# Kernel tuning notes

Hardware: AMD Instinct MI355X
Metric: run time of the kernel (lower is better)

The kernel has to match this reference:

```python
import jax, jax.numpy as jnp
import numpy as np

N = 30000      # nodes
E = 480000     # edges (no self loops; GATConv adds them)
IN = 256       # in_features
OUT = 128      # out_features == per-head channels (concat=False)
H = 4          # heads
NEG_SLOPE = 0.2


def setup_inputs() -> dict:
    key = jax.random.key(0)
    k = jax.random.split(key, 6)
    x = jax.random.normal(k[0], (N, IN), dtype=jnp.float32)
    src = jax.random.randint(k[1], (E,), 0, N, dtype=jnp.int32)
    # guarantee no self loops (GATConv would strip them before re-adding)
    off = jax.random.randint(k[2], (E,), 1, N, dtype=jnp.int32)
    dst = (src + off) % N
    edge_index = jnp.stack([src, dst])  # [2, E]
    W = jax.random.normal(k[3], (IN, H * OUT), dtype=jnp.float32) / np.float32(np.sqrt(IN))
    att_src = jax.random.normal(k[4], (H, OUT), dtype=jnp.float32) / np.float32(np.sqrt(OUT))
    att_dst = jax.random.normal(k[5], (H, OUT), dtype=jnp.float32) / np.float32(np.sqrt(OUT))
    bias = jnp.zeros((OUT,), dtype=jnp.float32)
    return {"x": x, "edge_index": edge_index, "W": W,
            "att_src": att_src, "att_dst": att_dst, "bias": bias}


def reference(x, edge_index, W, att_src, att_dst, bias):
    n = x.shape[0]
    # dense projection -> per-head features [N, H, C]
    h = (x @ W).reshape(n, H, OUT)
    a_s = jnp.einsum('nhc,hc->nh', h, att_src)  # [N, H]
    a_d = jnp.einsum('nhc,hc->nh', h, att_dst)  # [N, H]
    # add self loops (GATConv default add_self_loops=True)
    loop = jnp.arange(n, dtype=edge_index.dtype)
    src = jnp.concatenate([edge_index[0], loop])  # [Et]
    dst = jnp.concatenate([edge_index[1], loop])  # [Et]
    # per-edge attention logits + LeakyReLU
    alpha = jax.nn.leaky_relu(a_s[src] + a_d[dst], NEG_SLOPE)  # [Et, H]
    # segment softmax over incoming edges of each dst node
    amax = jax.ops.segment_max(alpha, dst, num_segments=n)      # [N, H]
    ex = jnp.exp(alpha - amax[dst])
    denom = jax.ops.segment_sum(ex, dst, num_segments=n)        # [N, H]
    w = ex / denom[dst]                                          # [Et, H]
    # gather source features, weight, scatter-add to dst
    msg = h[src] * w[:, :, None]                                 # [Et, H, C]
    out = jax.ops.segment_sum(msg, dst, num_segments=n)          # [N, H, C]
    # concat=False -> mean over heads, then bias, then module's tanh
    out = out.mean(axis=1) + bias                                # [N, C]
    return jnp.tanh(out)
```

## Files before the change

### kernel.cpp

```cpp
#include <hip/hip_runtime.h>
#include <math.h>

#define IN_F   256
#define OUT_F  128
#define HEADS  4
#define HD     (HEADS * OUT_F)
#define K2     1024
#define NEG    0.2f
#define CAP    64

typedef __attribute__((ext_vector_type(8))) short short8;
typedef __attribute__((ext_vector_type(4))) float f32x4;

typedef __attribute__((address_space(1))) const void* gp_t;
typedef __attribute__((address_space(3))) void* lp_t;

static __device__ __forceinline__ ushort f2bf(float f) {
    union { float f; unsigned u; } v; v.f = f;
    unsigned r = (v.u + 0x7FFFu + ((v.u >> 16) & 1u)) >> 16;
    return (ushort)r;
}
static __device__ __forceinline__ float bflo(unsigned u) {
    union { unsigned u; float f; } v; v.u = u << 16; return v.f;
}
static __device__ __forceinline__ float bfhi(unsigned u) {
    union { unsigned u; float f; } v; v.u = u & 0xFFFF0000u; return v.f;
}

__global__ __launch_bounds__(256) void prep(const float* __restrict__ W,
                                            const float* __restrict__ att_src,
                                            const float* __restrict__ att_dst,
                                            const int* __restrict__ src,
                                            const int* __restrict__ dst,
                                            ushort* __restrict__ WT2,
                                            float* __restrict__ va_s,
                                            float* __restrict__ va_d,
                                            int* __restrict__ cursor,
                                            int* __restrict__ table,
                                            int n_edges) {
    const int b = blockIdx.x;
    const int tid = threadIdx.x;
    if (b < 512) {
        int idx = b * 256 + tid;
        int cout = idx >> 10, kk = idx & 1023;
        int h = kk >> 8, c = kk & 255;
        WT2[idx] = f2bf(W[(size_t)c * HD + h * OUT_F + cout]);
    } else if (b < 768) {
        const int lane = tid & 63;
        const int p = (b - 512) * 4 + (tid >> 6);
        const int h = p >> 8;
        const int k = p & 255;
        const float* wr = W + (size_t)k * HD + h * OUT_F;
        float w0 = wr[lane], w1 = wr[lane + 64];
        float s0 = att_src[h * OUT_F + lane], s1 = att_src[h * OUT_F + lane + 64];
        float d0 = att_dst[h * OUT_F + lane], d1 = att_dst[h * OUT_F + lane + 64];
        float ss = w0 * s0 + w1 * s1;
        float sd = w0 * d0 + w1 * d1;
#pragma unroll
        for (int off = 32; off > 0; off >>= 1) {
            ss += __shfl_xor(ss, off, 64);
            sd += __shfl_xor(sd, off, 64);
        }
        if (lane == 0) { va_s[p] = ss; va_d[p] = sd; }
    } else {
        int e = (b - 768) * 256 + tid;
        if (e < n_edges) {
            int d = dst[e];
            int r = atomicAdd(&cursor[d], 1);
            if (r < CAP) table[(size_t)d * CAP + r] = src[e];
        }
    }
}

__global__ __launch_bounds__(256) void fused_x(const float* __restrict__ X,
                                               const float* __restrict__ va_s,
                                               const float* __restrict__ va_d,
                                               ushort* __restrict__ Xb,
                                               float* __restrict__ a_s,
                                               float* __restrict__ a_d,
                                               int n_nodes) {
    const int lane = threadIdx.x & 63;
    const int node = blockIdx.x * 4 + (threadIdx.x >> 6);
    if (node >= n_nodes) return;
    float4 v = *(const float4*)(X + (size_t)node * IN_F + lane * 4);
    ushort4 o; o.x = f2bf(v.x); o.y = f2bf(v.y); o.z = f2bf(v.z); o.w = f2bf(v.w);
    *(ushort4*)(Xb + (size_t)node * IN_F + lane * 4) = o;

    float ps[HEADS], pd[HEADS];
#pragma unroll
    for (int hd = 0; hd < HEADS; ++hd) {
        float4 s4 = *(const float4*)(va_s + hd * IN_F + lane * 4);
        float4 d4 = *(const float4*)(va_d + hd * IN_F + lane * 4);
        ps[hd] = v.x * s4.x + v.y * s4.y + v.z * s4.z + v.w * s4.w;
        pd[hd] = v.x * d4.x + v.y * d4.y + v.z * d4.z + v.w * d4.w;
    }
#pragma unroll
    for (int off = 32; off > 0; off >>= 1) {
#pragma unroll
        for (int hd = 0; hd < HEADS; ++hd) {
            ps[hd] += __shfl_xor(ps[hd], off, 64);
            pd[hd] += __shfl_xor(pd[hd], off, 64);
        }
    }
    if (lane == 0) {
        float4 s4 = make_float4(ps[0], ps[1], ps[2], ps[3]);
        float4 d4 = make_float4(pd[0], pd[1], pd[2], pd[3]);
        *(float4*)(a_s + node * 4) = s4;
        *(float4*)(a_d + node * 4) = d4;
    }
}

#define ACC8(U, WE)                                                         \
    {                                                                       \
        float f0 = bflo((U).x), f1 = bfhi((U).x);                           \
        float f2 = bflo((U).y), f3 = bfhi((U).y);                           \
        acc[0][0] = fmaf((WE).x, f0, acc[0][0]);                            \
        acc[0][1] = fmaf((WE).x, f1, acc[0][1]);                            \
        acc[0][2] = fmaf((WE).x, f2, acc[0][2]);                            \
        acc[0][3] = fmaf((WE).x, f3, acc[0][3]);                            \
        acc[1][0] = fmaf((WE).y, f0, acc[1][0]);                            \
        acc[1][1] = fmaf((WE).y, f1, acc[1][1]);                            \
        acc[1][2] = fmaf((WE).y, f2, acc[1][2]);                            \
        acc[1][3] = fmaf((WE).y, f3, acc[1][3]);                            \
        acc[2][0] = fmaf((WE).z, f0, acc[2][0]);                            \
        acc[2][1] = fmaf((WE).z, f1, acc[2][1]);                            \
        acc[2][2] = fmaf((WE).z, f2, acc[2][2]);                            \
        acc[2][3] = fmaf((WE).z, f3, acc[2][3]);                            \
        acc[3][0] = fmaf((WE).w, f0, acc[3][0]);                            \
        acc[3][1] = fmaf((WE).w, f1, acc[3][1]);                            \
        acc[3][2] = fmaf((WE).w, f2, acc[3][2]);                            \
        acc[3][3] = fmaf((WE).w, f3, acc[3][3]);                            \
    }

#define GATHER8(E, D0, D1, D2, D3, D4, D5, D6, D7)                          \
    {                                                                       \
        int t0 = __shfl(sreg, (E) + 0, 64);                                 \
        int t1 = __shfl(sreg, (E) + 1, 64);                                 \
        int t2 = __shfl(sreg, (E) + 2, 64);                                 \
        int t3 = __shfl(sreg, (E) + 3, 64);                                 \
        int t4 = __shfl(sreg, (E) + 4, 64);                                 \
        int t5 = __shfl(sreg, (E) + 5, 64);                                 \
        int t6 = __shfl(sreg, (E) + 6, 64);                                 \
        int t7 = __shfl(sreg, (E) + 7, 64);                                 \
        D0 = xb2[(size_t)t0 * 64 + lane];                                   \
        D1 = xb2[(size_t)t1 * 64 + lane];                                   \
        D2 = xb2[(size_t)t2 * 64 + lane];                                   \
        D3 = xb2[(size_t)t3 * 64 + lane];                                   \
        D4 = xb2[(size_t)t4 * 64 + lane];                                   \
        D5 = xb2[(size_t)t5 * 64 + lane];                                   \
        D6 = xb2[(size_t)t6 * 64 + lane];                                   \
        D7 = xb2[(size_t)t7 * 64 + lane];                                   \
    }

__global__ __launch_bounds__(256) void gat_agg(const ushort* __restrict__ Xb,
                                               const float* __restrict__ a_s,
                                               const float* __restrict__ a_d,
                                               const int* __restrict__ cursor,
                                               const int* __restrict__ table,
                                               ushort* __restrict__ Zb,
                                               int n_nodes) {
    __shared__ float4 wse[4][CAP];
    const int lane = threadIdx.x & 63;
    const int wid  = threadIdx.x >> 6;
    int n = blockIdx.x * 4 + wid;
    const bool valid = n < n_nodes;
    if (!valid) n = n_nodes - 1;
    int deg = cursor[n]; if (deg > CAP) deg = CAP;
    const int* row = table + (size_t)n * CAP;
    const bool act = lane < deg;
    int sreg = act ? row[lane] : n;

    const uint2* xb2 = (const uint2*)Xb;
    uint2 uself = xb2[(size_t)n * 64 + lane];

    const int ngroups = (deg + 7) >> 3;
    uint2 ua0, ua1, ua2, ua3, ua4, ua5, ua6, ua7;
    if (ngroups > 0) GATHER8(0, ua0, ua1, ua2, ua3, ua4, ua5, ua6, ua7);

    const float4 ad4 = *(const float4*)(a_d + n * 4);
    const float4 as4 = *(const float4*)(a_s + n * 4);
    const float ad[4] = {ad4.x, ad4.y, ad4.z, ad4.w};
    float aself[4];
    {
        const float asn[4] = {as4.x, as4.y, as4.z, as4.w};
#pragma unroll
        for (int hd = 0; hd < 4; ++hd) {
            float al0 = asn[hd] + ad[hd];
            aself[hd] = al0 > 0.f ? al0 : NEG * al0;
        }
    }
    float al[4];
    {
        float4 av = *(const float4*)(a_s + (size_t)sreg * 4);
        const float as_[4] = {av.x, av.y, av.z, av.w};
#pragma unroll
        for (int hd = 0; hd < 4; ++hd) {
            float a = as_[hd] + ad[hd];
            a = a > 0.f ? a : NEG * a;
            al[hd] = act ? a : -1e30f;
        }
    }
    float m[4];
#pragma unroll
    for (int hd = 0; hd < 4; ++hd) m[hd] = al[hd];
#pragma unroll
    for (int off = 32; off > 0; off >>= 1)
#pragma unroll
        for (int hd = 0; hd < 4; ++hd)
            m[hd] = fmaxf(m[hd], __shfl_xor(m[hd], off, 64));
#pragma unroll
    for (int hd = 0; hd < 4; ++hd) m[hd] = fmaxf(m[hd], aself[hd]);

    float w[4], den[4];
#pragma unroll
    for (int hd = 0; hd < 4; ++hd) {
        w[hd] = act ? __expf(al[hd] - m[hd]) : 0.f;
        den[hd] = w[hd];
    }
#pragma unroll
    for (int off = 32; off > 0; off >>= 1)
#pragma unroll
        for (int hd = 0; hd < 4; ++hd)
            den[hd] += __shfl_xor(den[hd], off, 64);

    float es[4], rdv[4];
#pragma unroll
    for (int hd = 0; hd < 4; ++hd) {
        es[hd] = __expf(aself[hd] - m[hd]);
        rdv[hd] = 1.f / (den[hd] + es[hd]);
    }

    wse[wid][lane] = make_float4(w[0], w[1], w[2], w[3]);
    __syncthreads();

    float acc[4][4];
    {
        float f0 = bflo(uself.x), f1 = bfhi(uself.x);
        float f2 = bflo(uself.y), f3 = bfhi(uself.y);
#pragma unroll
        for (int hd = 0; hd < 4; ++hd) {
            acc[hd][0] = es[hd] * f0;
            acc[hd][1] = es[hd] * f1;
            acc[hd][2] = es[hd] * f2;
            acc[hd][3] = es[hd] * f3;
        }
    }
#pragma unroll 1
    for (int g = 0; g < ngroups; ++g) {
        int e = g * 8;
        uint2 ub0, ub1, ub2, ub3, ub4, ub5, ub6, ub7;
        if (g + 1 < ngroups)
            GATHER8(e + 8, ub0, ub1, ub2, ub3, ub4, ub5, ub6, ub7);
        float4 w0 = wse[wid][e + 0]; float4 w1 = wse[wid][e + 1];
        float4 w2 = wse[wid][e + 2]; float4 w3 = wse[wid][e + 3];
        float4 w4 = wse[wid][e + 4]; float4 w5 = wse[wid][e + 5];
        float4 w6 = wse[wid][e + 6]; float4 w7 = wse[wid][e + 7];
        ACC8(ua0, w0); ACC8(ua1, w1); ACC8(ua2, w2); ACC8(ua3, w3);
        ACC8(ua4, w4); ACC8(ua5, w5); ACC8(ua6, w6); ACC8(ua7, w7);
        if (g + 1 < ngroups) {
            ua0 = ub0; ua1 = ub1; ua2 = ub2; ua3 = ub3;
            ua4 = ub4; ua5 = ub5; ua6 = ub6; ua7 = ub7;
        }
    }

    if (valid) {
        ushort* zr = Zb + (size_t)n * K2;
#pragma unroll
        for (int hd = 0; hd < 4; ++hd) {
            ushort4 z;
            z.x = f2bf(acc[hd][0] * rdv[hd]);
            z.y = f2bf(acc[hd][1] * rdv[hd]);
            z.z = f2bf(acc[hd][2] * rdv[hd]);
            z.w = f2bf(acc[hd][3] * rdv[hd]);
            *(ushort4*)(zr + hd * 256 + lane * 4) = z;
        }
    }
}

#define GBM 64
#define GBN 128
#define GBK 64

__global__ __launch_bounds__(256) void gemm2(const ushort* __restrict__ Zb,
                                             const ushort* __restrict__ WT2,
                                             const float* __restrict__ bias,
                                             float* __restrict__ out,
                                             int n_nodes) {
    __shared__ ushort As[GBM][GBK];
    __shared__ ushort Bs[GBN][GBK];
    const int tid = threadIdx.x;
    const int m0 = blockIdx.y * GBM;
    const int wave = tid >> 6, lane = tid & 63;
    const int wm = (wave & 1) * 32, wn = (wave >> 1) * 64;
    const int l15 = lane & 15, quad = lane >> 4;

    const int rr8 = lane >> 3;
    const int cg  = (lane & 7) ^ rr8;
    const ushort* gA0 = Zb + (size_t)(m0 + wave * 16 + rr8) * K2 + cg * 8;
    const ushort* gA1 = gA0 + 8 * K2;
    const ushort* gB0 = WT2 + (size_t)(wave * 32 + rr8) * K2 + cg * 8;
    const ushort* gB1 = gB0 + 8 * K2;
    const ushort* gB2 = gB0 + 16 * K2;
    const ushort* gB3 = gB0 + 24 * K2;
    ushort* lA0 = &As[wave * 16][0];
    ushort* lA1 = &As[wave * 16 + 8][0];
    ushort* lB0 = &Bs[wave * 32][0];
    ushort* lB1 = &Bs[wave * 32 + 8][0];
    ushort* lB2 = &Bs[wave * 32 + 16][0];
    ushort* lB3 = &Bs[wave * 32 + 24][0];

    f32x4 acc[2][4];
#pragma unroll
    for (int i = 0; i < 2; ++i)
#pragma unroll
        for (int j = 0; j < 4; ++j) acc[i][j] = (f32x4){0.f, 0.f, 0.f, 0.f};

    for (int k0 = 0; k0 < K2; k0 += GBK) {
        __syncthreads();
        __builtin_amdgcn_global_load_lds((gp_t)(gA0 + k0), (lp_t)lA0, 16, 0, 0);
        __builtin_amdgcn_global_load_lds((gp_t)(gA1 + k0), (lp_t)lA1, 16, 0, 0);
        __builtin_amdgcn_global_load_lds((gp_t)(gB0 + k0), (lp_t)lB0, 16, 0, 0);
        __builtin_amdgcn_global_load_lds((gp_t)(gB1 + k0), (lp_t)lB1, 16, 0, 0);
        __builtin_amdgcn_global_load_lds((gp_t)(gB2 + k0), (lp_t)lB2, 16, 0, 0);
        __builtin_amdgcn_global_load_lds((gp_t)(gB3 + k0), (lp_t)lB3, 16, 0, 0);
        __syncthreads();

#pragma unroll
        for (int t = 0; t < 2; ++t) {
            const int sl = ((t * 4 + quad) ^ (l15 & 7)) * 8;
            short8 af[2], bf_[4];
#pragma unroll
            for (int fm = 0; fm < 2; ++fm)
                af[fm] = *(const short8*)&As[wm + fm * 16 + l15][sl];
#pragma unroll
            for (int fn = 0; fn < 4; ++fn)
                bf_[fn] = *(const short8*)&Bs[wn + fn * 16 + l15][sl];
#pragma unroll
            for (int fm = 0; fm < 2; ++fm)
#pragma unroll
                for (int fn = 0; fn < 4; ++fn)
                    acc[fm][fn] = __builtin_amdgcn_mfma_f32_16x16x32_bf16(
                        af[fm], bf_[fn], acc[fm][fn], 0, 0, 0);
        }
    }

    float bcol[4];
#pragma unroll
    for (int fn = 0; fn < 4; ++fn) bcol[fn] = bias[wn + fn * 16 + l15];

#pragma unroll
    for (int fm = 0; fm < 2; ++fm) {
        int gmb = m0 + wm + fm * 16 + quad * 4;
#pragma unroll
        for (int reg = 0; reg < 4; ++reg) {
            int gm = gmb + reg;
            if (gm < n_nodes) {
#pragma unroll
                for (int fn = 0; fn < 4; ++fn) {
                    float o = tanhf(0.25f * acc[fm][fn][reg] + bcol[fn]);
                    out[(size_t)gm * OUT_F + wn + fn * 16 + l15] = o;
                }
            }
        }
    }
}

extern "C" void kernel_launch(void* const* d_in, const int* in_sizes, int n_in,
                              void* d_out, int out_size, void* d_ws, size_t ws_size,
                              hipStream_t stream) {
    const float* x       = (const float*)d_in[0];
    const int*   ei      = (const int*)d_in[1];
    const float* W       = (const float*)d_in[2];
    const float* att_src = (const float*)d_in[3];
    const float* att_dst = (const float*)d_in[4];
    const float* bias    = (const float*)d_in[5];
    float* out = (float*)d_out;

    const int n_nodes = in_sizes[0] / IN_F;
    const int n_edges = in_sizes[1] / 2;
    const int* src = ei;
    const int* dst = ei + n_edges;

    char* ws = (char*)d_ws;
    size_t off = 0;
    auto alloc = [&](size_t bytes) -> void* {
        void* p = ws + off;
        off = (off + bytes + 255) & ~(size_t)255;
        return p;
    };
    ushort* Xb     = (ushort*)alloc((size_t)n_nodes * IN_F * sizeof(ushort));
    ushort* Zb     = (ushort*)alloc((size_t)n_nodes * K2 * sizeof(ushort));
    ushort* WT2    = (ushort*)alloc((size_t)OUT_F * K2 * sizeof(ushort));
    float*  va_s   = (float*)alloc((size_t)HEADS * IN_F * sizeof(float));
    float*  va_d   = (float*)alloc((size_t)HEADS * IN_F * sizeof(float));
    float*  a_s    = (float*)alloc((size_t)n_nodes * HEADS * sizeof(float));
    float*  a_d    = (float*)alloc((size_t)n_nodes * HEADS * sizeof(float));
    int*    cursor = (int*)alloc((size_t)n_nodes * sizeof(int));
    int*    table  = (int*)alloc((size_t)n_nodes * CAP * sizeof(int));
    (void)ws_size; (void)n_in; (void)out_size;

    hipMemsetAsync(cursor, 0, (size_t)n_nodes * sizeof(int), stream);

    const int nebk = (n_edges + 255) / 256;
    prep<<<768 + nebk, 256, 0, stream>>>(W, att_src, att_dst, src, dst,
                                         WT2, va_s, va_d, cursor, table, n_edges);
    fused_x<<<(n_nodes + 3) / 4, 256, 0, stream>>>(x, va_s, va_d, Xb, a_s, a_d, n_nodes);
    gat_agg<<<(n_nodes + 3) / 4, 256, 0, stream>>>(Xb, a_s, a_d, cursor, table,
                                                   Zb, n_nodes);

    dim3 ggrid(1, (n_nodes + GBM - 1) / GBM);
    gemm2<<<ggrid, 256, 0, stream>>>(Zb, WT2, bias, out, n_nodes);
}
```

Measured before the change: 206.6 us.

## Stage neighbor gathers through LDS and double-buffer the second GEMM

The aggregation kernel now gathers neighbor feature rows straight into shared memory with async global-to-LDS loads. These loads are double-buffered across 8-edge tiles, and the accumulation uses packed FP32 FMA instructions with pre-duplicated attention weights. The gemm2 kernel becomes a two-stage ping-pong pipeline with manual vmcnt waits and barriers, so the next K tile loads while the current one is computed. The aim is to hide gather and tile-load latency and cut VALU instruction count, at the cost of more LDS per block and hand-tuned wait counts that are fragile. Out-of-range waves now return early instead of being clamped.

```diff
diff --git a/kernel.cpp b/kernel.cpp
--- a/kernel.cpp
+++ b/kernel.cpp
@@ -11,6 +11,7 @@
 
 typedef __attribute__((ext_vector_type(8))) short short8;
 typedef __attribute__((ext_vector_type(4))) float f32x4;
+typedef __attribute__((ext_vector_type(2))) float f32x2;
 
 typedef __attribute__((address_space(1))) const void* gp_t;
 typedef __attribute__((address_space(3))) void* lp_t;
@@ -26,6 +27,8 @@
 static __device__ __forceinline__ float bfhi(unsigned u) {
     union { unsigned u; float f; } v; v.u = u & 0xFFFF0000u; return v.f;
 }
+
+#define PKFMA(D, A, B) asm("v_pk_fma_f32 %0, %1, %2, %0" : "+v"(D) : "v"(A), "v"(B))
 
 __global__ __launch_bounds__(256) void prep(const float* __restrict__ W,
                                             const float* __restrict__ att_src,
@@ -110,46 +113,44 @@
     }
 }
 
-#define ACC8(U, WE)                                                         \
+#define EDGE(E8)                                                            \
     {                                                                       \
-        float f0 = bflo((U).x), f1 = bfhi((U).x);                           \
-        float f2 = bflo((U).y), f3 = bfhi((U).y);                           \
-        acc[0][0] = fmaf((WE).x, f0, acc[0][0]);                            \
-        acc[0][1] = fmaf((WE).x, f1, acc[0][1]);                            \
-        acc[0][2] = fmaf((WE).x, f2, acc[0][2]);                            \
-        acc[0][3] = fmaf((WE).x, f3, acc[0][3]);                            \
-        acc[1][0] = fmaf((WE).y, f0, acc[1][0]);                            \
-        acc[1][1] = fmaf((WE).y, f1, acc[1][1]);                            \
-        acc[1][2] = fmaf((WE).y, f2, acc[1][2]);                            \
-        acc[1][3] = fmaf((WE).y, f3, acc[1][3]);                            \
-        acc[2][0] = fmaf((WE).z, f0, acc[2][0]);                            \
-        acc[2][1] = fmaf((WE).z, f1, acc[2][1]);                            \
-        acc[2][2] = fmaf((WE).z, f2, acc[2][2]);                            \
-        acc[2][3] = fmaf((WE).z, f3, acc[2][3]);                            \
-        acc[3][0] = fmaf((WE).w, f0, acc[3][0]);                            \
-        acc[3][1] = fmaf((WE).w, f1, acc[3][1]);                            \
-        acc[3][2] = fmaf((WE).w, f2, acc[3][2]);                            \
-        acc[3][3] = fmaf((WE).w, f3, acc[3][3]);                            \
-    }
-
-#define GATHER8(E, D0, D1, D2, D3, D4, D5, D6, D7)                          \
+        uint2 u = *(const uint2*)(cons + (E8) * 512);                       \
+        float4 wA = *(const float4*)(wp + (E8) * 8);                        \
+        float4 wB = *(const float4*)(wp + (E8) * 8 + 4);                    \
+        f32x2 f01 = {bflo(u.x), bfhi(u.x)};                                 \
+        f32x2 f23 = {bflo(u.y), bfhi(u.y)};                                 \
+        f32x2 w0p = {wA.x, wA.y}, w1p = {wA.z, wA.w};                       \
+        f32x2 w2p = {wB.x, wB.y}, w3p = {wB.z, wB.w};                       \
+        PKFMA(a01[0], f01, w0p); PKFMA(a23[0], f23, w0p);                   \
+        PKFMA(a01[1], f01, w1p); PKFMA(a23[1], f23, w1p);                   \
+        PKFMA(a01[2], f01, w2p); PKFMA(a23[2], f23, w2p);                   \
+        PKFMA(a01[3], f01, w3p); PKFMA(a23[3], f23, w3p);                   \
+    }
+
+#define ISSUE(EB, DST)                                                      \
     {                                                                       \
-        int t0 = __shfl(sreg, (E) + 0, 64);                                 \
-        int t1 = __shfl(sreg, (E) + 1, 64);                                 \
-        int t2 = __shfl(sreg, (E) + 2, 64);                                 \
-        int t3 = __shfl(sreg, (E) + 3, 64);                                 \
-        int t4 = __shfl(sreg, (E) + 4, 64);                                 \
-        int t5 = __shfl(sreg, (E) + 5, 64);                                 \
-        int t6 = __shfl(sreg, (E) + 6, 64);                                 \
-        int t7 = __shfl(sreg, (E) + 7, 64);                                 \
-        D0 = xb2[(size_t)t0 * 64 + lane];                                   \
-        D1 = xb2[(size_t)t1 * 64 + lane];                                   \
-        D2 = xb2[(size_t)t2 * 64 + lane];                                   \
-        D3 = xb2[(size_t)t3 * 64 + lane];                                   \
-        D4 = xb2[(size_t)t4 * 64 + lane];                                   \
-        D5 = xb2[(size_t)t5 * 64 + lane];                                   \
-        D6 = xb2[(size_t)t6 * 64 + lane];                                   \
-        D7 = xb2[(size_t)t7 * 64 + lane];                                   \
+        asm volatile("s_waitcnt lgkmcnt(0)" ::: "memory");                  \
+        int s0_ = __shfl(sreg, (EB) + 0, 64);                               \
+        int s1_ = __shfl(sreg, (EB) + 1, 64);                               \
+        int s2_ = __shfl(sreg, (EB) + 2, 64);                               \
+        int s3_ = __shfl(sreg, (EB) + 3, 64);                               \
+        int s4_ = __shfl(sreg, (EB) + 4, 64);                               \
+        int s5_ = __shfl(sreg, (EB) + 5, 64);                               \
+        int s6_ = __shfl(sreg, (EB) + 6, 64);                               \
+        int s7_ = __shfl(sreg, (EB) + 7, 64);                               \
+        int sa_ = (lane & 32) ? s1_ : s0_;                                  \
+        int sb_ = (lane & 32) ? s3_ : s2_;                                  \
+        int sc_ = (lane & 32) ? s5_ : s4_;                                  \
+        int sd_ = (lane & 32) ? s7_ : s6_;                                  \
+        __builtin_amdgcn_global_load_lds((gp_t)(xb16 + (size_t)sa_ * 256),  \
+                                         (lp_t)((DST) + 0 * 1024), 16, 0, 0);\
+        __builtin_amdgcn_global_load_lds((gp_t)(xb16 + (size_t)sb_ * 256),  \
+                                         (lp_t)((DST) + 1 * 1024), 16, 0, 0);\
+        __builtin_amdgcn_global_load_lds((gp_t)(xb16 + (size_t)sc_ * 256),  \
+                                         (lp_t)((DST) + 2 * 1024), 16, 0, 0);\
+        __builtin_amdgcn_global_load_lds((gp_t)(xb16 + (size_t)sd_ * 256),  \
+                                         (lp_t)((DST) + 3 * 1024), 16, 0, 0);\
     }
 
 __global__ __launch_bounds__(256) void gat_agg(const ushort* __restrict__ Xb,
@@ -159,23 +160,23 @@
                                                const int* __restrict__ table,
                                                ushort* __restrict__ Zb,
                                                int n_nodes) {
-    __shared__ float4 wse[4][CAP];
+    __shared__ ushort xst[4][2][8][256];
+    __shared__ f32x2 wse2[4][CAP][4];
     const int lane = threadIdx.x & 63;
     const int wid  = threadIdx.x >> 6;
-    int n = blockIdx.x * 4 + wid;
-    const bool valid = n < n_nodes;
-    if (!valid) n = n_nodes - 1;
+    const int n = blockIdx.x * 4 + wid;
+    if (n >= n_nodes) return;
     int deg = cursor[n]; if (deg > CAP) deg = CAP;
     const int* row = table + (size_t)n * CAP;
     const bool act = lane < deg;
     int sreg = act ? row[lane] : n;
 
+    const ushort* xb16 = Xb + (lane & 31) * 8;
     const uint2* xb2 = (const uint2*)Xb;
     uint2 uself = xb2[(size_t)n * 64 + lane];
 
-    const int ngroups = (deg + 7) >> 3;
-    uint2 ua0, ua1, ua2, ua3, ua4, ua5, ua6, ua7;
-    if (ngroups > 0) GATHER8(0, ua0, ua1, ua2, ua3, ua4, ua5, ua6, ua7);
+    const int ntiles = (deg + 7) >> 3;
+    if (ntiles > 0) ISSUE(0, (char*)&xst[wid][0][0][0]);
 
     const float4 ad4 = *(const float4*)(a_d + n * 4);
     const float4 as4 = *(const float4*)(a_s + n * 4);
@@ -230,50 +231,44 @@
         rdv[hd] = 1.f / (den[hd] + es[hd]);
     }
 
-    wse[wid][lane] = make_float4(w[0], w[1], w[2], w[3]);
-    __syncthreads();
-
-    float acc[4][4];
+    *(float4*)&wse2[wid][lane][0] = make_float4(w[0], w[0], w[1], w[1]);
+    *(float4*)&wse2[wid][lane][2] = make_float4(w[2], w[2], w[3], w[3]);
+
+    f32x2 a01[4], a23[4];
     {
-        float f0 = bflo(uself.x), f1 = bfhi(uself.x);
-        float f2 = bflo(uself.y), f3 = bfhi(uself.y);
+        f32x2 s01 = {bflo(uself.x), bfhi(uself.x)};
+        f32x2 s23 = {bflo(uself.y), bfhi(uself.y)};
 #pragma unroll
         for (int hd = 0; hd < 4; ++hd) {
-            acc[hd][0] = es[hd] * f0;
-            acc[hd][1] = es[hd] * f1;
-            acc[hd][2] = es[hd] * f2;
-            acc[hd][3] = es[hd] * f3;
+            f32x2 eh = {es[hd], es[hd]};
+            a01[hd] = s01 * eh;
+            a23[hd] = s23 * eh;
         }
     }
 #pragma unroll 1
-    for (int g = 0; g < ngroups; ++g) {
-        int e = g * 8;
-        uint2 ub0, ub1, ub2, ub3, ub4, ub5, ub6, ub7;
-        if (g + 1 < ngroups)
-            GATHER8(e + 8, ub0, ub1, ub2, ub3, ub4, ub5, ub6, ub7);
-        float4 w0 = wse[wid][e + 0]; float4 w1 = wse[wid][e + 1];
-        float4 w2 = wse[wid][e + 2]; float4 w3 = wse[wid][e + 3];
-        float4 w4 = wse[wid][e + 4]; float4 w5 = wse[wid][e + 5];
-        float4 w6 = wse[wid][e + 6]; float4 w7 = wse[wid][e + 7];
-        ACC8(ua0, w0); ACC8(ua1, w1); ACC8(ua2, w2); ACC8(ua3, w3);
-        ACC8(ua4, w4); ACC8(ua5, w5); ACC8(ua6, w6); ACC8(ua7, w7);
-        if (g + 1 < ngroups) {
-            ua0 = ub0; ua1 = ub1; ua2 = ub2; ua3 = ub3;
-            ua4 = ub4; ua5 = ub5; ua6 = ub6; ua7 = ub7;
-        }
-    }
-
-    if (valid) {
-        ushort* zr = Zb + (size_t)n * K2;
-#pragma unroll
-        for (int hd = 0; hd < 4; ++hd) {
-            ushort4 z;
-            z.x = f2bf(acc[hd][0] * rdv[hd]);
-            z.y = f2bf(acc[hd][1] * rdv[hd]);
-            z.z = f2bf(acc[hd][2] * rdv[hd]);
-            z.w = f2bf(acc[hd][3] * rdv[hd]);
-            *(ushort4*)(zr + hd * 256 + lane * 4) = z;
-        }
+    for (int t = 0; t < ntiles; ++t) {
+        if (t + 1 < ntiles) {
+            ISSUE((t + 1) * 8, (char*)&xst[wid][(t + 1) & 1][0][0]);
+            asm volatile("s_waitcnt vmcnt(4)" ::: "memory");
+        } else {
+            asm volatile("s_waitcnt vmcnt(0)" ::: "memory");
+        }
+        const char* cons = (const char*)&xst[wid][t & 1][0][0] + lane * 8;
+        const float* wp = (const float*)&wse2[wid][t * 8][0];
+        EDGE(0); EDGE(1); EDGE(2); EDGE(3);
+        EDGE(4); EDGE(5); EDGE(6); EDGE(7);
+    }
+
+    ushort* zr = Zb + (size_t)n * K2;
+#pragma unroll
+    for (int hd = 0; hd < 4; ++hd) {
+        f32x2 r2 = {rdv[hd], rdv[hd]};
+        f32x2 z01 = a01[hd] * r2;
+        f32x2 z23 = a23[hd] * r2;
+        ushort4 z;
+        z.x = f2bf(z01.x); z.y = f2bf(z01.y);
+        z.z = f2bf(z23.x); z.w = f2bf(z23.y);
+        *(ushort4*)(zr + hd * 256 + lane * 4) = z;
     }
 }
 
@@ -286,8 +281,8 @@
                                              const float* __restrict__ bias,
                                              float* __restrict__ out,
                                              int n_nodes) {
-    __shared__ ushort As[GBM][GBK];
-    __shared__ ushort Bs[GBN][GBK];
+    __shared__ ushort As[2][GBM][GBK];
+    __shared__ ushort Bs[2][GBN][GBK];
     const int tid = threadIdx.x;
     const int m0 = blockIdx.y * GBM;
     const int wave = tid >> 6, lane = tid & 63;
@@ -302,12 +297,23 @@
     const ushort* gB1 = gB0 + 8 * K2;
     const ushort* gB2 = gB0 + 16 * K2;
     const ushort* gB3 = gB0 + 24 * K2;
-    ushort* lA0 = &As[wave * 16][0];
-    ushort* lA1 = &As[wave * 16 + 8][0];
-    ushort* lB0 = &Bs[wave * 32][0];
-    ushort* lB1 = &Bs[wave * 32 + 8][0];
-    ushort* lB2 = &Bs[wave * 32 + 16][0];
-    ushort* lB3 = &Bs[wave * 32 + 24][0];
+
+#define STAGE(T, B)                                                          \
+    {                                                                        \
+        const int ko_ = (T) * GBK;                                           \
+        __builtin_amdgcn_global_load_lds((gp_t)(gA0 + ko_),                  \
+            (lp_t)&As[B][wave * 16][0], 16, 0, 0);                           \
+        __builtin_amdgcn_global_load_lds((gp_t)(gA1 + ko_),                  \
+            (lp_t)&As[B][wave * 16 + 8][0], 16, 0, 0);                       \
+        __builtin_amdgcn_global_load_lds((gp_t)(gB0 + ko_),                  \
+            (lp_t)&Bs[B][wave * 32][0], 16, 0, 0);                           \
+        __builtin_amdgcn_global_load_lds((gp_t)(gB1 + ko_),                  \
+            (lp_t)&Bs[B][wave * 32 + 8][0], 16, 0, 0);                       \
+        __builtin_amdgcn_global_load_lds((gp_t)(gB2 + ko_),                  \
+            (lp_t)&Bs[B][wave * 32 + 16][0], 16, 0, 0);                      \
+        __builtin_amdgcn_global_load_lds((gp_t)(gB3 + ko_),                  \
+            (lp_t)&Bs[B][wave * 32 + 24][0], 16, 0, 0);                      \
+    }
 
     f32x4 acc[2][4];
 #pragma unroll
@@ -315,26 +321,29 @@
 #pragma unroll
         for (int j = 0; j < 4; ++j) acc[i][j] = (f32x4){0.f, 0.f, 0.f, 0.f};
 
-    for (int k0 = 0; k0 < K2; k0 += GBK) {
-        __syncthreads();
-        __builtin_amdgcn_global_load_lds((gp_t)(gA0 + k0), (lp_t)lA0, 16, 0, 0);
-        __builtin_amdgcn_global_load_lds((gp_t)(gA1 + k0), (lp_t)lA1, 16, 0, 0);
-        __builtin_amdgcn_global_load_lds((gp_t)(gB0 + k0), (lp_t)lB0, 16, 0, 0);
-        __builtin_amdgcn_global_load_lds((gp_t)(gB1 + k0), (lp_t)lB1, 16, 0, 0);
-        __builtin_amdgcn_global_load_lds((gp_t)(gB2 + k0), (lp_t)lB2, 16, 0, 0);
-        __builtin_amdgcn_global_load_lds((gp_t)(gB3 + k0), (lp_t)lB3, 16, 0, 0);
-        __syncthreads();
-
-#pragma unroll
-        for (int t = 0; t < 2; ++t) {
-            const int sl = ((t * 4 + quad) ^ (l15 & 7)) * 8;
+    const int NT = K2 / GBK;
+    STAGE(0, 0);
+#pragma unroll 1
+    for (int t = 0; t < NT; ++t) {
+        const int b = t & 1;
+        if (t + 1 < NT) {
+            STAGE(t + 1, b ^ 1);
+            asm volatile("s_waitcnt vmcnt(6)" ::: "memory");
+        } else {
+            asm volatile("s_waitcnt vmcnt(0)" ::: "memory");
+        }
+        asm volatile("s_barrier" ::: "memory");
+
+#pragma unroll
+        for (int tt = 0; tt < 2; ++tt) {
+            const int sl = ((tt * 4 + quad) ^ (l15 & 7)) * 8;
             short8 af[2], bf_[4];
 #pragma unroll
             for (int fm = 0; fm < 2; ++fm)
-                af[fm] = *(const short8*)&As[wm + fm * 16 + l15][sl];
+                af[fm] = *(const short8*)&As[b][wm + fm * 16 + l15][sl];
 #pragma unroll
             for (int fn = 0; fn < 4; ++fn)
-                bf_[fn] = *(const short8*)&Bs[wn + fn * 16 + l15][sl];
+                bf_[fn] = *(const short8*)&Bs[b][wn + fn * 16 + l15][sl];
 #pragma unroll
             for (int fm = 0; fm < 2; ++fm)
 #pragma unroll
@@ -342,6 +351,7 @@
                     acc[fm][fn] = __builtin_amdgcn_mfma_f32_16x16x32_bf16(
                         af[fm], bf_[fn], acc[fm][fn], 0, 0, 0);
         }
+        asm volatile("s_barrier" ::: "memory");
     }
 
     float bcol[4];
```

New measurement: 195.3 us. -5.5%, faster.
